# Optimization experiments

Measured on AMD Instinct MI355X. Metric: run time of the kernel, lower is better.

Reference implementation:

```python
import jax, jax.numpy as jnp
import numpy as np

B, N, C, H, D, K = 4, 8192, 384, 12, 2, 256
M = N // K          # 32 members per cluster
CH = C // H         # 32 head dim


def setup_inputs() -> dict:
    key = jax.random.key(0)
    ks = jax.random.split(key, 8)
    pos = jax.random.uniform(ks[0], (B, N, D), jnp.float32) * 100.0
    feat = jax.random.normal(ks[1], (B, N, C), jnp.float32)
    # each batch's points partitioned into K clusters of M members (a permutation)
    perms = jax.vmap(lambda kk: jax.random.permutation(kk, N))(jax.random.split(ks[2], B))
    member_idx = perms.reshape(B * K, M).astype(jnp.int32)               # z x m
    batch_idx = jnp.broadcast_to(
        jnp.repeat(jnp.arange(B, dtype=jnp.int32), K)[:, None], (B * K, M))
    w = 0.02
    qkv_w = jax.random.normal(ks[3], (3 * C, C), jnp.float32) * w
    qkv_b = jnp.zeros((3 * C,), jnp.float32)
    pos_w = jax.random.normal(ks[4], (H, D), jnp.float32) * w
    pos_b = jnp.zeros((H,), jnp.float32)
    proj_w = jax.random.normal(ks[5], (C, C), jnp.float32) * w
    proj_b = jnp.zeros((C,), jnp.float32)
    return dict(pos=pos, feat=feat, member_idx=member_idx, batch_idx=batch_idx,
                qkv_w=qkv_w, qkv_b=qkv_b, pos_w=pos_w, pos_b=pos_b,
                proj_w=proj_w, proj_b=proj_b, k=K)


def reference(pos, feat, member_idx, batch_idx, qkv_w, qkv_b, pos_w, pos_b,
              proj_w, proj_b, k):
    # attend_means=True, mask=None, cluster_score=None, q_subsample_idx=None path
    b, n, c = feat.shape
    d = pos.shape[2]
    h = pos_w.shape[0]
    ch = c // h
    z, m = member_idx.shape
    scale = ch ** -0.5

    qkv = feat @ qkv_w.T + qkv_b            # b,n,3c
    q = qkv[..., :c]                        # b,n,c
    kv = qkv[..., c:]                       # b,n,2c

    pos_orig = pos
    pos_n = pos / jnp.max(pos.reshape(-1, d), axis=0)   # per-coordinate max norm

    # irregular gather of kv / pos per cluster member
    kv_g = kv[batch_idx, member_idx]        # z,m,2c
    pos_g = pos_n[batch_idx, member_idx]    # z,m,d

    # cluster_score=None, mask=None -> uniform weights 1/m (mean over members)
    kv_mean = jnp.mean(kv_g, axis=1).reshape(b, k, 2, h, ch)
    pos_mean = jnp.mean(pos_g, axis=1).reshape(b, k, d)

    key_ = kv_mean[:, :, 0].transpose(0, 2, 1, 3)   # b,h,k,ch
    v = kv_mean[:, :, 1].transpose(0, 2, 1, 3)      # b,h,k,ch
    qh = q.reshape(b, n, h, ch).transpose(0, 2, 1, 3) * scale  # b,h,n,ch

    attn = jnp.einsum('bhnc,bhkc->bhnk', qh, key_)  # b,h,n,k
    rel_pos = pos_mean[:, None, :, :] - pos_orig[:, :, None, :]  # b,n,k,d
    pos_bias = jnp.einsum('bnkd,hd->bhnk', rel_pos, pos_w) + pos_b[None, :, None, None]
    attn = jax.nn.softmax(attn + pos_bias, axis=-1)

    out = jnp.einsum('bhnk,bhkc->bnhc', attn, v).reshape(b, n, c)
    return out @ proj_w.T + proj_b
```

## Files before the change

kernel.cpp:

```cpp
#include <hip/hip_runtime.h>

typedef __attribute__((ext_vector_type(8))) short bf16x8;
typedef __attribute__((ext_vector_type(4))) float f32x4;

#define MFMA16(a,b,c) __builtin_amdgcn_mfma_f32_16x16x32_bf16((a),(b),(c),0,0,0)

__device__ __forceinline__ float b2f(unsigned short u){
  union { unsigned u; float f; } x; x.u = ((unsigned)u) << 16; return x.f;
}
__device__ __forceinline__ unsigned short f2b(float f){
  union { float f; unsigned u; } x; x.f = f;
  unsigned r = x.u + 0x7FFFu + ((x.u >> 16) & 1u);
  return (unsigned short)(r >> 16);
}
__device__ __forceinline__ unsigned pk_rne(float a, float b){
  unsigned ua = __float_as_uint(a), ub = __float_as_uint(b);
  ua += 0x7FFFu + ((ua >> 16) & 1u);
  ub += 0x7FFFu + ((ub >> 16) & 1u);
  return __builtin_amdgcn_perm(ub, ua, 0x07060302u);
}
__device__ __forceinline__ unsigned pk_trunc(float a, float b){
  return __builtin_amdgcn_perm(__float_as_uint(b), __float_as_uint(a), 0x07060302u);
}
__device__ __forceinline__ bf16x8 mk8(unsigned a, unsigned b, unsigned c, unsigned d){
  union { uint4 u; bf16x8 h; } x; x.u = make_uint4(a,b,c,d); return x.h;
}
__device__ __forceinline__ int permp(int cl){
  return (cl & 0xE0) | (((cl >> 2) & 3) << 3) | (((cl >> 4) & 1) << 2) | (cl & 3);
}

typedef __attribute__((address_space(3))) unsigned int lds_u32;
typedef const __attribute__((address_space(1))) unsigned int glb_u32;
__device__ __forceinline__ void gl_lds16(const void* g, void* l){
  __builtin_amdgcn_global_load_lds((glb_u32*)g, (lds_u32*)l, 16, 0, 0);
}

__global__ __launch_bounds__(256) void cvt_kernel(const float* __restrict__ in,
                                                  unsigned short* __restrict__ o, long n8){
  long i = (long)blockIdx.x*256 + threadIdx.x;
  if (i >= n8) return;
  const float4* p = (const float4*)(in + i*8);
  float4 a = p[0], b = p[1];
  *(uint4*)(o + i*8) = make_uint4(pk_rne(a.x,a.y), pk_rne(a.z,a.w),
                                  pk_rne(b.x,b.y), pk_rne(b.z,b.w));
}

__global__ __launch_bounds__(256) void posmax_kernel(const float* __restrict__ pos,
                                                     unsigned* __restrict__ pmax){
  int i = blockIdx.x*256 + threadIdx.x;
  float4 v = ((const float4*)pos)[i];
  float m0 = fmaxf(v.x, v.z), m1 = fmaxf(v.y, v.w);
  #pragma unroll
  for (int off = 32; off >= 1; off >>= 1){
    m0 = fmaxf(m0, __shfl_xor(m0, off, 64));
    m1 = fmaxf(m1, __shfl_xor(m1, off, 64));
  }
  if ((threadIdx.x & 63) == 0){
    atomicMax(&pmax[0], __float_as_uint(m0));
    atomicMax(&pmax[1], __float_as_uint(m1));
  }
}

__global__ __launch_bounds__(192) void cluster_means_kernel(
    const float* __restrict__ feat, const float* __restrict__ pos,
    const int* __restrict__ member_idx, const int* __restrict__ batch_idx,
    unsigned short* __restrict__ fm, float* __restrict__ pm)
{
  int z = blockIdx.x, t = threadIdx.x;
  __shared__ int bases[32];
  if (t < 32) bases[t] = batch_idx[z*32 + t]*8192 + member_idx[z*32 + t];
  __syncthreads();
  float a0 = 0.f, a1 = 0.f, p = 0.f;
  for (int m = 0; m < 32; m++){
    const float* row = feat + (long)bases[m]*384;
    a0 += row[t];
    a1 += row[t+192];
    if (t < 2) p += pos[(long)bases[m]*2 + t];
  }
  fm[(long)z*384 + t]       = f2b(a0 * (1.f/32.f));
  fm[(long)z*384 + t + 192] = f2b(a1 * (1.f/32.f));
  if (t < 2) pm[z*2 + t] = p * (1.f/32.f);
}

__global__ __launch_bounds__(256) void bias_kernel(
    const float* __restrict__ pm, const float* __restrict__ pmaxf,
    const float* __restrict__ pos_w, const float* __restrict__ pos_b,
    unsigned short* __restrict__ wt)
{
  int idx = blockIdx.x*256 + threadIdx.x;
  int kc = idx & 255;
  int bh = idx >> 8;
  int h = bh % 12;
  float p0 = pm[((bh/12)*256 + kc)*2]   / pmaxf[0];
  float p1 = pm[((bh/12)*256 + kc)*2+1] / pmaxf[1];
  float bias = p0*pos_w[h*2] + p1*pos_w[h*2+1] + pos_b[h];
  wt[(bh << 8) + permp(kc)] = f2b(exp2f(bias * 1.44269504088896340f));
}

__global__ __launch_bounds__(256) void gemm_kv_kernel(
    const unsigned short* __restrict__ A, const unsigned short* __restrict__ W,
    const float* __restrict__ bias, unsigned short* __restrict__ kh,
    unsigned short* __restrict__ vt, const unsigned short* __restrict__ wt)
{
  __shared__ unsigned short As[64*64];
  __shared__ unsigned short Ws[128*64];
  const int N = 768, K = 384;
  int mt = blockIdx.x / 6, nt = blockIdx.x - mt*6;
  int m0 = mt << 6, n0 = nt << 7;
  int tid = threadIdx.x;
  int lane = tid & 63, wave = tid >> 6;
  int wr = (wave >> 1) << 5, wc = (wave & 1) << 6;
  int l15 = lane & 15, quad = lane >> 4;
  int sw = l15 & 7;
  int srow = tid >> 3, sc8 = tid & 7;

  f32x4 acc[2][4];
  #pragma unroll
  for (int i = 0; i < 2; i++)
    #pragma unroll
    for (int j = 0; j < 4; j++) acc[i][j] = (f32x4){0.f,0.f,0.f,0.f};

  for (int k0 = 0; k0 < K; k0 += 64){
    __syncthreads();
    #pragma unroll
    for (int it = 0; it < 2; it++){
      int r = srow + it*32;
      int gc8 = sc8 ^ (r & 7);
      gl_lds16(A + (long)(m0+r)*K + k0 + gc8*8, As + it*2048 + wave*512);
    }
    #pragma unroll
    for (int it = 0; it < 4; it++){
      int r = srow + it*32;
      int gc8 = sc8 ^ (r & 7);
      gl_lds16(W + (long)(n0+r)*K + k0 + gc8*8, Ws + it*2048 + wave*512);
    }
    __syncthreads();
    #pragma unroll
    for (int kk = 0; kk < 2; kk++){
      bf16x8 af[2], bfr[4];
      #pragma unroll
      for (int i = 0; i < 2; i++)
        af[i] = *(const bf16x8*)(As + (wr + i*16 + l15)*64 + (((kk<<2)+quad) ^ sw)*8);
      #pragma unroll
      for (int j = 0; j < 4; j++)
        bfr[j] = *(const bf16x8*)(Ws + (wc + j*16 + l15)*64 + (((kk<<2)+quad) ^ sw)*8);
      #pragma unroll
      for (int i = 0; i < 2; i++)
        #pragma unroll
        for (int j = 0; j < 4; j++)
          acc[i][j] = MFMA16(af[i], bfr[j], acc[i][j]);
    }
  }

  #pragma unroll
  for (int j = 0; j < 4; j++){
    int col = n0 + wc + j*16 + l15;
    float bv = bias[col];
    #pragma unroll
    for (int i = 0; i < 2; i++){
      int row0 = m0 + wr + i*16 + quad*4;
      #pragma unroll
      for (int r = 0; r < 4; r++){
        float v = acc[i][j][r] + bv;
        int row = row0 + r;
        int b = row >> 8, cl = row & 255;
        if (col < 384){
          int h = col >> 5, ch = col & 31;
          kh[((((long)b*12 + h)*256 + cl)*32) + ch] = f2b(v);
        } else {
          int cn = col - 384;
          int h = cn >> 5, ch = cn & 31;
          int pp = permp(cl);
          int c8 = (pp >> 3) ^ (ch & 7);
          float w = b2f(wt[(((long)b*12 + h) << 8) + pp]);
          vt[(((long)b*12 + h)*32 + ch)*256 + c8*8 + (pp & 7)] = f2b(v * w);
        }
      }
    }
  }
}

template<int OUT_F32, int AF32>
__global__ __launch_bounds__(256) void gemm_fn_kernel(
    const void* __restrict__ Av, const unsigned short* __restrict__ W,
    const float* __restrict__ bias, void* __restrict__ Cv, float out_scale)
{
  __shared__ unsigned short As[64*72];
  __shared__ unsigned short Ws[384*64];
  const int K = 384, N = 384;
  int m0 = blockIdx.x << 6;
  int tid = threadIdx.x;
  int lane = tid & 63, wave = tid >> 6;
  int l15 = lane & 15, quad = lane >> 4;
  int sw = l15 & 7;
  int srow = tid >> 3, sc8 = tid & 7;

  f32x4 acc[4][6];
  #pragma unroll
  for (int i = 0; i < 4; i++)
    #pragma unroll
    for (int j = 0; j < 6; j++) acc[i][j] = (f32x4){0.f,0.f,0.f,0.f};

  for (int k0 = 0; k0 < K; k0 += 64){
    __syncthreads();
    if (AF32){
      const float* Af = (const float*)Av;
      #pragma unroll
      for (int it = 0; it < 4; it++){
        int r = (tid >> 4) + it*16;
        int c4 = tid & 15;
        float4 v = *(const float4*)(Af + (long)(m0+r)*K + k0 + c4*4);
        *(uint2*)(As + r*72 + c4*4) = make_uint2(pk_rne(v.x,v.y), pk_rne(v.z,v.w));
      }
    } else {
      const unsigned short* A = (const unsigned short*)Av;
      #pragma unroll
      for (int it = 0; it < 2; it++){
        int r = srow + it*32;
        int gc8 = sc8 ^ (r & 7);
        gl_lds16(A + (long)(m0+r)*K + k0 + gc8*8, As + it*2048 + wave*512);
      }
    }
    #pragma unroll
    for (int it = 0; it < 12; it++){
      int r = srow + it*32;
      int gc8 = sc8 ^ (r & 7);
      gl_lds16(W + (long)r*K + k0 + gc8*8, Ws + it*2048 + wave*512);
    }
    __syncthreads();
    #pragma unroll
    for (int kk = 0; kk < 2; kk++){
      bf16x8 af[4];
      #pragma unroll
      for (int i = 0; i < 4; i++){
        int r = i*16 + l15;
        if (AF32) af[i] = *(const bf16x8*)(As + r*72 + ((kk<<2)+quad)*8);
        else      af[i] = *(const bf16x8*)(As + r*64 + (((kk<<2)+quad) ^ sw)*8);
      }
      #pragma unroll
      for (int j = 0; j < 6; j++){
        bf16x8 bfr = *(const bf16x8*)(Ws + (wave*96 + j*16 + l15)*64 + (((kk<<2)+quad) ^ sw)*8);
        #pragma unroll
        for (int i = 0; i < 4; i++)
          acc[i][j] = MFMA16(af[i], bfr, acc[i][j]);
      }
    }
  }

  #pragma unroll
  for (int j = 0; j < 6; j++){
    int col = wave*96 + j*16 + l15;
    float bv = bias[col];
    #pragma unroll
    for (int i = 0; i < 4; i++){
      int row0 = m0 + i*16 + quad*4;
      #pragma unroll
      for (int r = 0; r < 4; r++){
        float v = (acc[i][j][r] + bv) * out_scale;
        if (OUT_F32) ((float*)Cv)[(long)(row0+r)*N + col] = v;
        else ((unsigned short*)Cv)[(long)(row0+r)*N + col] = f2b(v);
      }
    }
  }
}

__global__ __launch_bounds__(256) void attn_kernel(
    const unsigned short* __restrict__ qs,
    const unsigned short* __restrict__ kh,
    const unsigned short* __restrict__ vt,
    const unsigned short* __restrict__ wt,
    unsigned short* __restrict__ ao)
{
  __shared__ unsigned short keyS[256*32];
  __shared__ unsigned short vTS[32*256];
  __shared__ unsigned short wS[256];

  int bid = blockIdx.x;
  int chunk = bid & 127;
  int h = (bid >> 7) % 12;
  int b = bid / (128*12);
  int bh = b*12 + h;
  int n0 = chunk << 6;
  int tid = threadIdx.x, lane = tid & 63, wave = tid >> 6;
  int l15 = lane & 15, quad = lane >> 4;
  int sw = l15 & 7;

  const unsigned short* khb = kh + (long)bh*8192;
  const unsigned short* vtb = vt + (long)bh*8192;
  #pragma unroll
  for (int it = 0; it < 4; it++){
    gl_lds16(khb + it*2048 + tid*8, keyS + it*2048 + wave*512);
    gl_lds16(vtb + it*2048 + tid*8, vTS  + it*2048 + wave*512);
  }
  if (tid < 32) *(uint4*)(wS + tid*8) = *(const uint4*)(wt + ((long)bh << 8) + tid*8);
  __syncthreads();

  int tok0 = n0 + wave*16;
  bf16x8 aq = *(const bf16x8*)(qs + ((long)b*8192 + tok0 + l15)*384 + h*32 + quad*8);

  f32x4 S[16];
  #pragma unroll
  for (int kb = 0; kb < 16; kb++){
    bf16x8 bk = *(const bf16x8*)(keyS + (kb*16 + l15)*32 + quad*8);
    f32x4 z = {0.f,0.f,0.f,0.f};
    S[kb] = MFMA16(bk, aq, z);
  }

  #pragma unroll
  for (int kb = 0; kb < 16; kb++)
    #pragma unroll
    for (int c = 0; c < 4; c++) S[kb][c] = exp2f(S[kb][c]);

  f32x4 o0 = {0.f,0.f,0.f,0.f}, o1 = {0.f,0.f,0.f,0.f}, os = {0.f,0.f,0.f,0.f};
  #pragma unroll
  for (int ks = 0; ks < 8; ks++){
    bf16x8 pf = mk8(pk_trunc(S[2*ks][0],   S[2*ks][1]),
                    pk_trunc(S[2*ks][2],   S[2*ks][3]),
                    pk_trunc(S[2*ks+1][0], S[2*ks+1][1]),
                    pk_trunc(S[2*ks+1][2], S[2*ks+1][3]));
    int c8 = (4*ks + quad) ^ sw;
    bf16x8 a0 = *(const bf16x8*)(vTS + l15*256      + c8*8);
    bf16x8 a1 = *(const bf16x8*)(vTS + (16+l15)*256 + c8*8);
    bf16x8 wf = *(const bf16x8*)(wS + ks*32 + quad*8);
    o0 = MFMA16(a0, pf, o0);
    o1 = MFMA16(a1, pf, o1);
    os = MFMA16(wf, pf, os);
  }
  float inv = 1.f / os[0];
  long obase = ((long)b*8192 + tok0 + l15)*384 + h*32 + quad*4;
  unsigned q0 = pk_rne(o0[0]*inv, o0[1]*inv), q1 = pk_rne(o0[2]*inv, o0[3]*inv);
  unsigned q2 = pk_rne(o1[0]*inv, o1[1]*inv), q3 = pk_rne(o1[2]*inv, o1[3]*inv);
  *(uint2*)(ao + obase)      = make_uint2(q0, q1);
  *(uint2*)(ao + obase + 16) = make_uint2(q2, q3);
}

extern "C" void kernel_launch(void* const* d_in, const int* in_sizes, int n_in,
                              void* d_out, int out_size, void* d_ws, size_t ws_size,
                              hipStream_t stream)
{
  const float* pos      = (const float*)d_in[0];
  const float* feat     = (const float*)d_in[1];
  const int* member_idx = (const int*)d_in[2];
  const int* batch_idx  = (const int*)d_in[3];
  const float* qkv_w    = (const float*)d_in[4];
  const float* qkv_b    = (const float*)d_in[5];
  const float* pos_w    = (const float*)d_in[6];
  const float* pos_b    = (const float*)d_in[7];
  const float* proj_w   = (const float*)d_in[8];
  const float* proj_b   = (const float*)d_in[9];
  float* out = (float*)d_out;

  char* ws = (char*)d_ws;
  float* pmax           = (float*)ws;
  float* pm             = (float*)(ws + 256);
  unsigned short* fm    = (unsigned short*)(ws + 8704);
  unsigned short* kh    = (unsigned short*)(ws + 795136);
  unsigned short* vt    = (unsigned short*)(ws + 1581568);
  unsigned short* wt    = (unsigned short*)(ws + 2368000);
  unsigned short* q_s   = (unsigned short*)(ws + 2417152);
  unsigned short* ao    = (unsigned short*)(ws + 27582976);
  unsigned short* qkvwb = (unsigned short*)(ws + 52748800);
  unsigned short* projwb= (unsigned short*)(ws + 53633536);

  hipMemsetAsync(pmax, 0, 8, stream);
  posmax_kernel<<<64, 256, 0, stream>>>(pos, (unsigned*)pmax);
  cvt_kernel<<<216, 256, 0, stream>>>(qkv_w, qkvwb, 55296);
  cvt_kernel<<<72, 256, 0, stream>>>(proj_w, projwb, 18432);
  cluster_means_kernel<<<1024, 192, 0, stream>>>(feat, pos, member_idx, batch_idx, fm, pm);
  bias_kernel<<<48, 256, 0, stream>>>(pm, pmax, pos_w, pos_b, wt);
  gemm_kv_kernel<<<96, 256, 0, stream>>>(fm, qkvwb + 384*384, qkv_b + 384, kh, vt, wt);
  gemm_fn_kernel<0,1><<<512, 256, 0, stream>>>(feat, qkvwb, qkv_b, q_s,
                                               0.17677669529663687f * 1.44269504088896340f);
  attn_kernel<<<6144, 256, 0, stream>>>(q_s, kh, vt, wt, ao);
  gemm_fn_kernel<1,0><<<512, 256, 0, stream>>>(ao, projwb, proj_b, out, 1.0f);
}
```

Before: 226.1 us.

## Vectorize cluster-mean gather and double waves per block in row GEMMs

The cluster-means kernel now handles two clusters per 192-thread block, with each thread loading a float4 of the gathered feature row and writing packed bf16 pairs. The Q and output-projection GEMMs move to 512-thread blocks with 8 waves, each computing 48 output columns instead of 96, and the tile-staging loads are remapped across the extra threads. The aim is to widen memory accesses in the gather and to raise wave count and latency hiding in the GEMMs. In exchange, each wave reuses its A fragments across fewer columns and more waves compete for the same LDS tile.

```diff
diff --git a/kernel.cpp b/kernel.cpp
--- a/kernel.cpp
+++ b/kernel.cpp
@@ -66,20 +66,26 @@
     const int* __restrict__ member_idx, const int* __restrict__ batch_idx,
     unsigned short* __restrict__ fm, float* __restrict__ pm)
 {
-  int z = blockIdx.x, t = threadIdx.x;
-  __shared__ int bases[32];
-  if (t < 32) bases[t] = batch_idx[z*32 + t]*8192 + member_idx[z*32 + t];
+  int t = threadIdx.x;
+  int g = t / 96, tl = t - g*96;
+  int z = blockIdx.x*2 + g;
+  __shared__ int bases[2][32];
+  if (tl < 32) bases[g][tl] = batch_idx[z*32 + tl]*8192 + member_idx[z*32 + tl];
   __syncthreads();
-  float a0 = 0.f, a1 = 0.f, p = 0.f;
+  float4 a = {0.f,0.f,0.f,0.f};
+  float p = 0.f;
+  const float4* f4 = (const float4*)feat;
+  #pragma unroll 4
   for (int m = 0; m < 32; m++){
-    const float* row = feat + (long)bases[m]*384;
-    a0 += row[t];
-    a1 += row[t+192];
-    if (t < 2) p += pos[(long)bases[m]*2 + t];
-  }
-  fm[(long)z*384 + t]       = f2b(a0 * (1.f/32.f));
-  fm[(long)z*384 + t + 192] = f2b(a1 * (1.f/32.f));
-  if (t < 2) pm[z*2 + t] = p * (1.f/32.f);
+    int row = bases[g][m];
+    float4 v = f4[(long)row*96 + tl];
+    a.x += v.x; a.y += v.y; a.z += v.z; a.w += v.w;
+    if (tl < 2) p += pos[(long)row*2 + tl];
+  }
+  unsigned d0 = pk_rne(a.x*(1.f/32.f), a.y*(1.f/32.f));
+  unsigned d1 = pk_rne(a.z*(1.f/32.f), a.w*(1.f/32.f));
+  *(uint2*)(fm + (long)z*384 + tl*4) = make_uint2(d0, d1);
+  if (tl < 2) pm[z*2 + tl] = p * (1.f/32.f);
 }
 
 __global__ __launch_bounds__(256) void bias_kernel(
@@ -181,7 +187,7 @@
 }
 
 template<int OUT_F32, int AF32>
-__global__ __launch_bounds__(256) void gemm_fn_kernel(
+__global__ __launch_bounds__(512) void gemm_fn_kernel(
     const void* __restrict__ Av, const unsigned short* __restrict__ W,
     const float* __restrict__ bias, void* __restrict__ Cv, float out_scale)
 {
@@ -195,37 +201,30 @@
   int sw = l15 & 7;
   int srow = tid >> 3, sc8 = tid & 7;
 
-  f32x4 acc[4][6];
+  f32x4 acc[4][3];
   #pragma unroll
   for (int i = 0; i < 4; i++)
     #pragma unroll
-    for (int j = 0; j < 6; j++) acc[i][j] = (f32x4){0.f,0.f,0.f,0.f};
+    for (int j = 0; j < 3; j++) acc[i][j] = (f32x4){0.f,0.f,0.f,0.f};
 
   for (int k0 = 0; k0 < K; k0 += 64){
     __syncthreads();
     if (AF32){
       const float* Af = (const float*)Av;
-      #pragma unroll
-      for (int it = 0; it < 4; it++){
-        int r = (tid >> 4) + it*16;
-        int c4 = tid & 15;
-        float4 v = *(const float4*)(Af + (long)(m0+r)*K + k0 + c4*4);
-        *(uint2*)(As + r*72 + c4*4) = make_uint2(pk_rne(v.x,v.y), pk_rne(v.z,v.w));
-      }
+      const float4* src = (const float4*)(Af + (long)(m0+srow)*K + k0 + sc8*8);
+      float4 v0 = src[0], v1 = src[1];
+      *(uint4*)(As + srow*72 + sc8*8) = make_uint4(pk_rne(v0.x,v0.y), pk_rne(v0.z,v0.w),
+                                                   pk_rne(v1.x,v1.y), pk_rne(v1.z,v1.w));
     } else {
       const unsigned short* A = (const unsigned short*)Av;
-      #pragma unroll
-      for (int it = 0; it < 2; it++){
-        int r = srow + it*32;
-        int gc8 = sc8 ^ (r & 7);
-        gl_lds16(A + (long)(m0+r)*K + k0 + gc8*8, As + it*2048 + wave*512);
-      }
-    }
-    #pragma unroll
-    for (int it = 0; it < 12; it++){
-      int r = srow + it*32;
+      int gc8 = sc8 ^ (srow & 7);
+      gl_lds16(A + (long)(m0+srow)*K + k0 + gc8*8, As + wave*512);
+    }
+    #pragma unroll
+    for (int it = 0; it < 6; it++){
+      int r = it*64 + srow;
       int gc8 = sc8 ^ (r & 7);
-      gl_lds16(W + (long)r*K + k0 + gc8*8, Ws + it*2048 + wave*512);
+      gl_lds16(W + (long)r*K + k0 + gc8*8, Ws + it*4096 + wave*512);
     }
     __syncthreads();
     #pragma unroll
@@ -238,8 +237,8 @@
         else      af[i] = *(const bf16x8*)(As + r*64 + (((kk<<2)+quad) ^ sw)*8);
       }
       #pragma unroll
-      for (int j = 0; j < 6; j++){
-        bf16x8 bfr = *(const bf16x8*)(Ws + (wave*96 + j*16 + l15)*64 + (((kk<<2)+quad) ^ sw)*8);
+      for (int j = 0; j < 3; j++){
+        bf16x8 bfr = *(const bf16x8*)(Ws + (wave*48 + j*16 + l15)*64 + (((kk<<2)+quad) ^ sw)*8);
         #pragma unroll
         for (int i = 0; i < 4; i++)
           acc[i][j] = MFMA16(af[i], bfr, acc[i][j]);
@@ -248,8 +247,8 @@
   }
 
   #pragma unroll
-  for (int j = 0; j < 6; j++){
-    int col = wave*96 + j*16 + l15;
+  for (int j = 0; j < 3; j++){
+    int col = wave*48 + j*16 + l15;
     float bv = bias[col];
     #pragma unroll
     for (int i = 0; i < 4; i++){
@@ -366,11 +365,11 @@
   posmax_kernel<<<64, 256, 0, stream>>>(pos, (unsigned*)pmax);
   cvt_kernel<<<216, 256, 0, stream>>>(qkv_w, qkvwb, 55296);
   cvt_kernel<<<72, 256, 0, stream>>>(proj_w, projwb, 18432);
-  cluster_means_kernel<<<1024, 192, 0, stream>>>(feat, pos, member_idx, batch_idx, fm, pm);
+  cluster_means_kernel<<<512, 192, 0, stream>>>(feat, pos, member_idx, batch_idx, fm, pm);
   bias_kernel<<<48, 256, 0, stream>>>(pm, pmax, pos_w, pos_b, wt);
   gemm_kv_kernel<<<96, 256, 0, stream>>>(fm, qkvwb + 384*384, qkv_b + 384, kh, vt, wt);
-  gemm_fn_kernel<0,1><<<512, 256, 0, stream>>>(feat, qkvwb, qkv_b, q_s,
+  gemm_fn_kernel<0,1><<<512, 512, 0, stream>>>(feat, qkvwb, qkv_b, q_s,
                                                0.17677669529663687f * 1.44269504088896340f);
   attn_kernel<<<6144, 256, 0, stream>>>(q_s, kh, vt, wt, ao);
-  gemm_fn_kernel<1,0><<<512, 256, 0, stream>>>(ao, projwb, proj_b, out, 1.0f);
-}
+  gemm_fn_kernel<1,0><<<512, 512, 0, stream>>>(ao, projwb, proj_b, out, 1.0f);
+}
```

After: 224.8 us. Within noise of the previous version (-0.6%).
